# Kernel optimization log

Hardware: AMD Instinct MI355X
Metric: run time of the kernel (lower is better)

## Reference

```python
import jax, jax.numpy as jnp
import numpy as np

B, A, D, F, O, NB = 64, 1024, 5, 256, 256, 6  # batch, max_atoms, max_degree, ishape, oshape, bond feat dim


def setup_inputs() -> dict:
    key = jax.random.key(0)
    k1, k2, k3, k4 = jax.random.split(key, 4)
    atoms = jax.random.normal(k1, (B, A, F), dtype=jnp.float32)
    bonds = jax.random.normal(k2, (B, A, D, NB), dtype=jnp.float32)
    # -1 marks missing neighbor (degree padding); valid indices in [0, A)
    edges = jax.random.randint(k3, (B, A, D), -1, A)
    # xavier-normal-ish init for the 6 degree-specific weights, stacked [6, F+NB, O]
    scale = (2.0 / (F + NB + O)) ** 0.5
    degW = jax.random.normal(k4, (6, F + NB, O), dtype=jnp.float32) * scale
    b = jnp.full((1, O), 0.01, dtype=jnp.float32)
    return {"atoms": atoms, "bonds": bonds, "edges": edges, "degW": degW, "b": b}


def reference(atoms, bonds, edges, degW, b):
    # atoms: [B, A, F]; bonds: [B, A, D, NB]; edges: [B, A, D] int (-1 = pad)
    degrees = (edges != -1).sum(-1, keepdims=True)  # [B, A, 1]
    # pad a zero row at index 0 so edge -1 -> 0 gathers the mask value 0
    padded = jnp.pad(atoms, ((0, 0), (1, 0), (0, 0)))  # [B, A+1, F]
    neigh = jax.vmap(lambda p, e: p[e])(padded, edges + 1)  # [B, A, D, F]
    summed_atom = atoms + neigh.sum(axis=2)  # include_self=True
    feats = jnp.concatenate([summed_atom, bonds.sum(axis=2)], axis=-1)  # [B, A, F+NB]
    out = jnp.zeros((atoms.shape[0], atoms.shape[1], degW.shape[-1]), atoms.dtype)
    for d in range(6):  # fixed small structural loop over degree buckets
        mask = (degrees == d).astype(atoms.dtype)  # [B, A, 1]
        out = out + jax.nn.sigmoid(feats @ degW[d] + b) * mask
    return out
```

## Files before the change

### kernel.cpp

```cpp
#include <hip/hip_runtime.h>
#include <cstdint>

#define BATCH  64
#define NATOMS 1024
#define DEG    5
#define FIN    256
#define OOUT   256
#define NBF    6
#define KDIM   262
#define KP     288
#define NKT    9
#define MROWS  (BATCH * NATOMS)
#define MT     32
#define AS     296

typedef __attribute__((ext_vector_type(8))) short bf16x8;
typedef __attribute__((ext_vector_type(4))) float f32x4;

__device__ __forceinline__ unsigned short f2bf(float x) {
    unsigned u = __float_as_uint(x);
    u += 0x7fff + ((u >> 16) & 1);
    return (unsigned short)(u >> 16);
}
__device__ __forceinline__ float bf2f(unsigned short h) {
    return __uint_as_float(((unsigned)h) << 16);
}
__device__ __forceinline__ float sigmoidf_(float x) {
    return 1.f / (1.f + __expf(-x));
}

__global__ __launch_bounds__(256)
void convert_w_kernel(const float* __restrict__ degW, unsigned short* __restrict__ Wsw)
{
    const int idx = blockIdx.x * 256 + threadIdx.x;
    if (idx >= 16 * NKT * 64) return;
    const int lane = idx & 63;
    const int t    = (idx >> 6) % NKT;
    const int g    = (idx >> 6) / NKT;
    const int col  = g * 16 + (lane & 15);
    const int k0   = t * 32 + (lane >> 4) * 8;
    const float* __restrict__ W5 = degW + (size_t)DEG * KDIM * OOUT;
    unsigned short* dst = Wsw + (size_t)idx * 8;
    #pragma unroll
    for (int j = 0; j < 8; ++j) {
        const int k = k0 + j;
        dst[j] = f2bf((k < KDIM) ? W5[(size_t)k * OOUT + col] : 0.f);
    }
}

__global__ __launch_bounds__(256, 4)
void nfp_fused_kernel(const float* __restrict__ atoms, const float* __restrict__ bonds,
                      const int* __restrict__ edges, const unsigned short* __restrict__ Wsw,
                      const float* __restrict__ degW, const float* __restrict__ bias,
                      float* __restrict__ out)
{
    __shared__ short Afeat[MT * AS];
    __shared__ int   edg[MT * DEG];
    __shared__ int   deg_lds[MT];

    const int tid  = threadIdx.x;
    const int lane = tid & 63;
    const int wave = tid >> 6;

    const int bid   = blockIdx.x;
    const int xcd   = bid & 7;
    const int per   = bid >> 3;
    const int batch = (per >> 5) * 8 + xcd;
    const int blk   = per & 31;
    const int row0  = batch * NATOMS + blk * MT;

    if (tid < MT * DEG) edg[tid] = edges[row0 * DEG + tid];
    __syncthreads();
    if (tid < MT) {
        int dc = 0;
        #pragma unroll
        for (int d = 0; d < DEG; ++d) dc += (edg[tid * DEG + d] != -1) ? 1 : 0;
        deg_lds[tid] = dc;
    }

    const float* __restrict__ abase = atoms + ((size_t)batch << 10) * FIN;
    const int selfrow = blk * MT;
    #pragma unroll
    for (int c = 0; c < 4; ++c) {
        const int mb = wave * 8 + c * 2;
        float4 self[2];
        float4 nv[2][DEG];
        #pragma unroll
        for (int r = 0; r < 2; ++r) {
            const int m = mb + r;
            self[r] = *(const float4*)&abase[(size_t)(selfrow + m) * FIN + lane * 4];
            #pragma unroll
            for (int d = 0; d < DEG; ++d) {
                const int e  = edg[m * DEG + d];
                const int ei = (e >= 0) ? e : 0;
                nv[r][d] = *(const float4*)&abase[(size_t)ei * FIN + lane * 4];
            }
        }
        #pragma unroll
        for (int r = 0; r < 2; ++r) {
            const int m = mb + r;
            float4 v = self[r];
            #pragma unroll
            for (int d = 0; d < DEG; ++d) {
                const float fl = (edg[m * DEG + d] >= 0) ? 1.f : 0.f;
                v.x += fl * nv[r][d].x; v.y += fl * nv[r][d].y;
                v.z += fl * nv[r][d].z; v.w += fl * nv[r][d].w;
            }
            ushort4 us;
            us.x = f2bf(v.x); us.y = f2bf(v.y); us.z = f2bf(v.z); us.w = f2bf(v.w);
            *(ushort4*)&Afeat[m * AS + lane * 4] = us;
        }
    }
    #pragma unroll
    for (int i = lane; i < 8 * 32; i += 64) {
        const int r  = i >> 5, kk = i & 31;
        const int m  = wave * 8 + r;
        float bv = 0.f;
        if (kk < NBF) {
            const float* bb = bonds + ((size_t)row0 + m) * (DEG * NBF) + kk;
            bv = bb[0] + bb[NBF] + bb[2 * NBF] + bb[3 * NBF] + bb[4 * NBF];
        }
        Afeat[m * AS + FIN + kk] = f2bf(bv);
    }
    __syncthreads();

    const int fr = lane & 15;
    const int q  = lane >> 4;
    const int wn = wave * 64;

    f32x4 acc[2][4];
    #pragma unroll
    for (int i = 0; i < 2; ++i)
        #pragma unroll
        for (int j = 0; j < 4; ++j)
            acc[i][j] = (f32x4){0.f, 0.f, 0.f, 0.f};

    bf16x8 bcur[4], bnxt[4];
    #pragma unroll
    for (int j = 0; j < 4; ++j)
        bcur[j] = *(const bf16x8*)&Wsw[((size_t)((wave * 4 + j) * NKT) * 64 + lane) * 8];

    #pragma unroll
    for (int t = 0; t < NKT; ++t) {
        if (t + 1 < NKT) {
            #pragma unroll
            for (int j = 0; j < 4; ++j)
                bnxt[j] = *(const bf16x8*)&Wsw[((size_t)((wave * 4 + j) * NKT + t + 1) * 64 + lane) * 8];
        }
        bf16x8 af[2];
        #pragma unroll
        for (int i = 0; i < 2; ++i)
            af[i] = *(const bf16x8*)&Afeat[(i * 16 + fr) * AS + t * 32 + q * 8];
        #pragma unroll
        for (int i = 0; i < 2; ++i)
            #pragma unroll
            for (int j = 0; j < 4; ++j)
                acc[i][j] = __builtin_amdgcn_mfma_f32_16x16x32_bf16(af[i], bcur[j], acc[i][j], 0, 0, 0);
        #pragma unroll
        for (int j = 0; j < 4; ++j) bcur[j] = bnxt[j];
    }

    #pragma unroll
    for (int j = 0; j < 4; ++j) {
        const int gn = wn + j * 16 + fr;
        const float bj = bias[gn];
        #pragma unroll
        for (int i = 0; i < 2; ++i) {
            #pragma unroll
            for (int r = 0; r < 4; ++r) {
                const int lm = i * 16 + q * 4 + r;
                if (deg_lds[lm] == DEG)
                    __builtin_nontemporal_store(sigmoidf_(acc[i][j][r] + bj),
                                                &out[((size_t)row0 + lm) * OOUT + gn]);
            }
        }
    }

    for (int m = 0; m < MT; ++m) {
        const int dg = deg_lds[m];
        if (dg == DEG) continue;
        const float* __restrict__ W = degW + (size_t)dg * KDIM * OOUT;
        float s0 = 0.f, s1 = 0.f, s2 = 0.f, s3 = 0.f;
        #pragma unroll 2
        for (int k = 0; k < 260; k += 4) {
            const float w0 = W[(size_t)(k + 0) * OOUT + tid];
            const float w1 = W[(size_t)(k + 1) * OOUT + tid];
            const float w2 = W[(size_t)(k + 2) * OOUT + tid];
            const float w3 = W[(size_t)(k + 3) * OOUT + tid];
            s0 += bf2f(Afeat[m * AS + k + 0]) * w0;
            s1 += bf2f(Afeat[m * AS + k + 1]) * w1;
            s2 += bf2f(Afeat[m * AS + k + 2]) * w2;
            s3 += bf2f(Afeat[m * AS + k + 3]) * w3;
        }
        s0 += bf2f(Afeat[m * AS + 260]) * W[(size_t)260 * OOUT + tid];
        s1 += bf2f(Afeat[m * AS + 261]) * W[(size_t)261 * OOUT + tid];
        const float x = ((s0 + s1) + (s2 + s3)) + bias[tid];
        out[((size_t)row0 + m) * OOUT + tid] = sigmoidf_(x);
    }
}

#define FMT  32
#define FKT  32
#define FKPAD 288
__global__ __launch_bounds__(256, 2)
void nfp_conv_fallback(const float* __restrict__ atoms, const float* __restrict__ bonds,
                       const int* __restrict__ edges, const float* __restrict__ degW,
                       const float* __restrict__ bias, float* __restrict__ out)
{
    __shared__ float feats[FMT * FKPAD];
    __shared__ float wtile[FKT * OOUT];
    __shared__ int   edg[FMT * DEG];
    __shared__ int   deg_lds[FMT];
    __shared__ int   odd_list[FMT];
    __shared__ int   odd_cnt;
    __shared__ float b_lds[OOUT];

    const int tid = threadIdx.x, bid = blockIdx.x;
    const int batch = bid >> 5, a0 = (bid & 31) * FMT;
    const size_t atom_base = (size_t)batch * NATOMS;

    b_lds[tid] = bias[tid];
    if (tid == 0) odd_cnt = 0;
    if (tid < FMT * DEG) {
        const int m = tid / DEG, d = tid % DEG;
        edg[tid] = edges[(atom_base + a0 + m) * DEG + d];
    }
    __syncthreads();
    if (tid < FMT) {
        int dc = 0;
        #pragma unroll
        for (int d = 0; d < DEG; ++d) dc += (edg[tid * DEG + d] != -1) ? 1 : 0;
        deg_lds[tid] = dc;
        if (dc != DEG) { const int idx = atomicAdd(&odd_cnt, 1); odd_list[idx] = tid; }
    }
    __syncthreads();
    {
        const int f = tid;
        for (int m = 0; m < FMT; ++m) {
            float v = atoms[(atom_base + a0 + m) * FIN + f];
            #pragma unroll
            for (int d = 0; d < DEG; ++d) {
                const int e = edg[m * DEG + d];
                if (e >= 0) v += atoms[(atom_base + e) * FIN + f];
            }
            feats[m * FKPAD + f] = v;
        }
        #pragma unroll
        for (int t = 0; t < 4; ++t) {
            const int idx = t * 256 + tid;
            const int m = idx >> 5, kk = idx & 31;
            float v = 0.f;
            if (kk < NBF) {
                const size_t bb = (atom_base + a0 + m) * (size_t)(DEG * NBF);
                #pragma unroll
                for (int d = 0; d < DEG; ++d) v += bonds[bb + d * NBF + kk];
            }
            feats[m * FKPAD + FIN + kk] = v;
        }
    }
    const float* __restrict__ W5 = degW + (size_t)DEG * KDIM * OOUT;
    float acc[4][8];
    #pragma unroll
    for (int i = 0; i < 4; ++i)
        #pragma unroll
        for (int j = 0; j < 8; ++j) acc[i][j] = 0.f;
    const int tx = tid & 31, ty = tid >> 5;
    for (int kt = 0; kt < FKPAD; kt += FKT) {
        __syncthreads();
        #pragma unroll
        for (int t = 0; t < FKT; ++t) {
            const int k = kt + t;
            wtile[t * OOUT + tid] = (k < KDIM) ? W5[(size_t)k * OOUT + tid] : 0.f;
        }
        __syncthreads();
        #pragma unroll 4
        for (int r = 0; r < FKT; ++r) {
            float a_frag[4];
            #pragma unroll
            for (int i = 0; i < 4; ++i) a_frag[i] = feats[(ty * 4 + i) * FKPAD + kt + r];
            float w_frag[8];
            #pragma unroll
            for (int j = 0; j < 8; ++j) w_frag[j] = wtile[r * OOUT + tx + j * 32];
            #pragma unroll
            for (int i = 0; i < 4; ++i)
                #pragma unroll
                for (int j = 0; j < 8; ++j) acc[i][j] += a_frag[i] * w_frag[j];
        }
    }
    #pragma unroll
    for (int i = 0; i < 4; ++i) {
        const int m = ty * 4 + i;
        if (deg_lds[m] == DEG) {
            const size_t row = (atom_base + a0 + m) * (size_t)OOUT;
            #pragma unroll
            for (int j = 0; j < 8; ++j) {
                const int o = tx + j * 32;
                out[row + o] = sigmoidf_(acc[i][j] + b_lds[o]);
            }
        }
    }
    const int ocnt = odd_cnt;
    for (int i = 0; i < ocnt; ++i) {
        const int m = odd_list[i], d = deg_lds[m];
        const float* __restrict__ W = degW + (size_t)d * KDIM * OOUT;
        float a2 = 0.f;
        for (int k = 0; k < KDIM; ++k) a2 += feats[m * FKPAD + k] * W[(size_t)k * OOUT + tid];
        const size_t row = (atom_base + a0 + m) * (size_t)OOUT;
        out[row + tid] = sigmoidf_(a2 + b_lds[tid]);
    }
}

extern "C" void kernel_launch(void* const* d_in, const int* in_sizes, int n_in,
                              void* d_out, int out_size, void* d_ws, size_t ws_size,
                              hipStream_t stream) {
    const float* atoms = (const float*)d_in[0];
    const float* bonds = (const float*)d_in[1];
    const int*   edges = (const int*)d_in[2];
    const float* degW  = (const float*)d_in[3];
    const float* bias  = (const float*)d_in[4];
    float* out = (float*)d_out;

    const size_t WSW_BYTES = (size_t)16 * NKT * 64 * 8 * 2;

    if (ws_size < WSW_BYTES) {
        nfp_conv_fallback<<<BATCH * (NATOMS / FMT), 256, 0, stream>>>(
            atoms, bonds, edges, degW, bias, out);
        return;
    }

    unsigned short* Wsw = (unsigned short*)d_ws;
    convert_w_kernel<<<(16 * NKT * 64 + 255) / 256, 256, 0, stream>>>(degW, Wsw);
    nfp_fused_kernel<<<MROWS / MT, 256, 0, stream>>>(
        atoms, bonds, edges, Wsw, degW, bias, out);
}
```

Before: 196.0 us.

## Run non-degree-5 rows through bf16 MFMA passes with all six weight sets

Converts all six degree weight matrices into swizzled bf16 MFMA fragments when workspace allows. Tiles that contain lower-degree atoms run an extra MFMA GEMM pass per present degree, replacing the per-row scalar fp32 fallback. The A-fragment loads from shared memory are also prefetched one k-step ahead. This adds a larger conversion kernel, bf16 rounding of the lower-degree weights, and redundant full-tile GEMMs for degrees that are rare.

After: 196.5 us. Within noise of the previous version (+0.3%).

```diff
diff --git a/kernel.cpp b/kernel.cpp
--- a/kernel.cpp
+++ b/kernel.cpp
@@ -8,12 +8,13 @@
 #define OOUT   256
 #define NBF    6
 #define KDIM   262
-#define KP     288
 #define NKT    9
 #define MROWS  (BATCH * NATOMS)
 #define MT     32
 #define AS     296
 
+#define FRAG_SHORTS (16 * NKT * 64 * 8)
+
 typedef __attribute__((ext_vector_type(8))) short bf16x8;
 typedef __attribute__((ext_vector_type(4))) float f32x4;
 
@@ -30,21 +31,26 @@
 }
 
 __global__ __launch_bounds__(256)
-void convert_w_kernel(const float* __restrict__ degW, unsigned short* __restrict__ Wsw)
+void convert_w_kernel(const float* __restrict__ degW, unsigned short* __restrict__ Wsw,
+                      int all6)
 {
+    const int total = (all6 ? 6 : 1) * 16 * NKT * 64;
     const int idx = blockIdx.x * 256 + threadIdx.x;
-    if (idx >= 16 * NKT * 64) return;
+    if (idx >= total) return;
     const int lane = idx & 63;
-    const int t    = (idx >> 6) % NKT;
-    const int g    = (idx >> 6) / NKT;
+    int r = idx >> 6;
+    const int t = r % NKT; r /= NKT;
+    const int g = r & 15;
+    const int d = r >> 4;
+    const int srcd = all6 ? d : DEG;
     const int col  = g * 16 + (lane & 15);
     const int k0   = t * 32 + (lane >> 4) * 8;
-    const float* __restrict__ W5 = degW + (size_t)DEG * KDIM * OOUT;
+    const float* __restrict__ W = degW + (size_t)srcd * KDIM * OOUT;
     unsigned short* dst = Wsw + (size_t)idx * 8;
     #pragma unroll
     for (int j = 0; j < 8; ++j) {
         const int k = k0 + j;
-        dst[j] = f2bf((k < KDIM) ? W5[(size_t)k * OOUT + col] : 0.f);
+        dst[j] = f2bf((k < KDIM) ? W[(size_t)k * OOUT + col] : 0.f);
     }
 }
 
@@ -52,11 +58,12 @@
 void nfp_fused_kernel(const float* __restrict__ atoms, const float* __restrict__ bonds,
                       const int* __restrict__ edges, const unsigned short* __restrict__ Wsw,
                       const float* __restrict__ degW, const float* __restrict__ bias,
-                      float* __restrict__ out)
+                      float* __restrict__ out, int all6)
 {
     __shared__ short Afeat[MT * AS];
     __shared__ int   edg[MT * DEG];
     __shared__ int   deg_lds[MT];
+    __shared__ int   degmask;
 
     const int tid  = threadIdx.x;
     const int lane = tid & 63;
@@ -69,6 +76,7 @@
     const int blk   = per & 31;
     const int row0  = batch * NATOMS + blk * MT;
 
+    if (tid == 0) degmask = 0;
     if (tid < MT * DEG) edg[tid] = edges[row0 * DEG + tid];
     __syncthreads();
     if (tid < MT) {
@@ -76,58 +84,127 @@
         #pragma unroll
         for (int d = 0; d < DEG; ++d) dc += (edg[tid * DEG + d] != -1) ? 1 : 0;
         deg_lds[tid] = dc;
+        atomicOr(&degmask, 1 << dc);
     }
 
     const float* __restrict__ abase = atoms + ((size_t)batch << 10) * FIN;
     const int selfrow = blk * MT;
-    #pragma unroll
-    for (int c = 0; c < 4; ++c) {
-        const int mb = wave * 8 + c * 2;
-        float4 self[2];
-        float4 nv[2][DEG];
-        #pragma unroll
-        for (int r = 0; r < 2; ++r) {
-            const int m = mb + r;
-            self[r] = *(const float4*)&abase[(size_t)(selfrow + m) * FIN + lane * 4];
-            #pragma unroll
-            for (int d = 0; d < DEG; ++d) {
-                const int e  = edg[m * DEG + d];
-                const int ei = (e >= 0) ? e : 0;
-                nv[r][d] = *(const float4*)&abase[(size_t)ei * FIN + lane * 4];
-            }
-        }
-        #pragma unroll
-        for (int r = 0; r < 2; ++r) {
-            const int m = mb + r;
-            float4 v = self[r];
-            #pragma unroll
-            for (int d = 0; d < DEG; ++d) {
-                const float fl = (edg[m * DEG + d] >= 0) ? 1.f : 0.f;
-                v.x += fl * nv[r][d].x; v.y += fl * nv[r][d].y;
-                v.z += fl * nv[r][d].z; v.w += fl * nv[r][d].w;
-            }
-            ushort4 us;
-            us.x = f2bf(v.x); us.y = f2bf(v.y); us.z = f2bf(v.z); us.w = f2bf(v.w);
-            *(ushort4*)&Afeat[m * AS + lane * 4] = us;
-        }
-    }
-    #pragma unroll
-    for (int i = lane; i < 8 * 32; i += 64) {
-        const int r  = i >> 5, kk = i & 31;
-        const int m  = wave * 8 + r;
-        float bv = 0.f;
-        if (kk < NBF) {
-            const float* bb = bonds + ((size_t)row0 + m) * (DEG * NBF) + kk;
-            bv = bb[0] + bb[NBF] + bb[2 * NBF] + bb[3 * NBF] + bb[4 * NBF];
-        }
-        Afeat[m * AS + FIN + kk] = f2bf(bv);
-    }
-    __syncthreads();
-
+    const int mw = wave * 8;
+
+#define GATHER_CHUNK(MB, NR)                                                          \
+    {                                                                                 \
+        float4 self[NR]; float4 nv[NR][DEG]; int msk[NR];                             \
+        _Pragma("unroll")                                                             \
+        for (int r = 0; r < NR; ++r) {                                                \
+            const int m = (MB) + r;                                                   \
+            msk[r] = 0;                                                               \
+            self[r] = *(const float4*)&abase[(size_t)(selfrow + m) * FIN + lane * 4]; \
+            _Pragma("unroll")                                                         \
+            for (int d = 0; d < DEG; ++d) {                                           \
+                const int e = edg[m * DEG + d];                                       \
+                msk[r] |= (e >= 0) ? (1 << d) : 0;                                    \
+                const int ei = (e >= 0) ? e : 0;          \
+                nv[r][d] = *(const float4*)&abase[(size_t)ei * FIN + lane * 4];       \
+            }                                                                         \
+        }                                                                             \
+        _Pragma("unroll")                                                             \
+        for (int r = 0; r < NR; ++r) {                                                \
+            const int m = (MB) + r;                                                   \
+            float4 v = self[r];                                                       \
+            _Pragma("unroll")                                                         \
+            for (int d = 0; d < DEG; ++d) {                                           \
+                const float fl = ((msk[r] >> d) & 1) ? 1.f : 0.f;                     \
+                v.x += fl * nv[r][d].x; v.y += fl * nv[r][d].y;                       \
+                v.z += fl * nv[r][d].z; v.w += fl * nv[r][d].w;                       \
+            }                                                                         \
+            ushort4 us;                                                               \
+            us.x = f2bf(v.x); us.y = f2bf(v.y); us.z = f2bf(v.z); us.w = f2bf(v.w);   \
+            *(ushort4*)&Afeat[m * AS + lane * 4] = us;                                \
+        }                                                                             \
+    }
+
+    GATHER_CHUNK(mw + 0, 3)
+    GATHER_CHUNK(mw + 3, 3)
+    GATHER_CHUNK(mw + 6, 2)
+#undef GATHER_CHUNK
+
+    {
+        const int mz = mw + (lane >> 3), pz = lane & 7;
+        ushort4 zz = {0, 0, 0, 0};
+        *(ushort4*)&Afeat[mz * AS + FIN + pz * 4] = zz;
+        if (lane < 48) {
+            const int r  = lane / 6;
+            const int kk = lane - r * 6;
+            const int m  = mw + r;
+            const float* __restrict__ bb = bonds + ((size_t)(row0 + m)) * (DEG * NBF) + kk;
+            const float bv = bb[0] + bb[NBF] + bb[2 * NBF] + bb[3 * NBF] + bb[4 * NBF];
+            Afeat[m * AS + FIN + kk] = f2bf(bv);
+        }
+    }
+
+    const unsigned short* __restrict__ Wb5 =
+        Wsw + (all6 ? (size_t)DEG * FRAG_SHORTS : (size_t)0);
     const int fr = lane & 15;
     const int q  = lane >> 4;
     const int wn = wave * 64;
 
+    bf16x8 b0[4];
+    #pragma unroll
+    for (int j = 0; j < 4; ++j)
+        b0[j] = *(const bf16x8*)&Wb5[((size_t)((wave * 4 + j) * NKT) * 64 + lane) * 8];
+
+    __syncthreads();
+
+    auto gemm_pass = [&](const unsigned short* __restrict__ Wb, bf16x8 (&bini)[4],
+                         f32x4 (&a)[2][4]) {
+        bf16x8 bcur[4], bnxt[4], acur[2], anxt[2];
+        #pragma unroll
+        for (int j = 0; j < 4; ++j) bcur[j] = bini[j];
+        #pragma unroll
+        for (int i = 0; i < 2; ++i)
+            acur[i] = *(const bf16x8*)&Afeat[(i * 16 + fr) * AS + q * 8];
+        #pragma unroll
+        for (int t = 0; t < NKT; ++t) {
+            if (t + 1 < NKT) {
+                #pragma unroll
+                for (int j = 0; j < 4; ++j)
+                    bnxt[j] = *(const bf16x8*)&Wb[((size_t)((wave * 4 + j) * NKT + t + 1) * 64 + lane) * 8];
+                #pragma unroll
+                for (int i = 0; i < 2; ++i)
+                    anxt[i] = *(const bf16x8*)&Afeat[(i * 16 + fr) * AS + (t + 1) * 32 + q * 8];
+            }
+            #pragma unroll
+            for (int i = 0; i < 2; ++i)
+                #pragma unroll
+                for (int j = 0; j < 4; ++j)
+                    a[i][j] = __builtin_amdgcn_mfma_f32_16x16x32_bf16(acur[i], bcur[j], a[i][j], 0, 0, 0);
+            if (t + 1 < NKT) {
+                #pragma unroll
+                for (int j = 0; j < 4; ++j) bcur[j] = bnxt[j];
+                #pragma unroll
+                for (int i = 0; i < 2; ++i) acur[i] = anxt[i];
+            }
+        }
+    };
+
+    auto epilogue = [&](f32x4 (&a)[2][4], int want) {
+        #pragma unroll
+        for (int j = 0; j < 4; ++j) {
+            const int gn = wn + j * 16 + fr;
+            const float bj = bias[gn];
+            #pragma unroll
+            for (int i = 0; i < 2; ++i) {
+                #pragma unroll
+                for (int r = 0; r < 4; ++r) {
+                    const int lm = i * 16 + q * 4 + r;
+                    if (deg_lds[lm] == want)
+                        __builtin_nontemporal_store(sigmoidf_(a[i][j][r] + bj),
+                                                    &out[((size_t)row0 + lm) * OOUT + gn]);
+                }
+            }
+        }
+    };
+
     f32x4 acc[2][4];
     #pragma unroll
     for (int i = 0; i < 2; ++i)
@@ -135,67 +212,52 @@
         for (int j = 0; j < 4; ++j)
             acc[i][j] = (f32x4){0.f, 0.f, 0.f, 0.f};
 
-    bf16x8 bcur[4], bnxt[4];
-    #pragma unroll
-    for (int j = 0; j < 4; ++j)
-        bcur[j] = *(const bf16x8*)&Wsw[((size_t)((wave * 4 + j) * NKT) * 64 + lane) * 8];
-
-    #pragma unroll
-    for (int t = 0; t < NKT; ++t) {
-        if (t + 1 < NKT) {
+    gemm_pass(Wb5, b0, acc);
+    epilogue(acc, DEG);
+
+    int dmask = degmask & 0x1F;
+    if (dmask == 0) return;
+
+    if (all6) {
+        while (dmask) {
+            const int d = __ffs(dmask) - 1;
+            dmask &= dmask - 1;
+            const unsigned short* __restrict__ Wd = Wsw + (size_t)d * FRAG_SHORTS;
+            bf16x8 bd[4];
             #pragma unroll
             for (int j = 0; j < 4; ++j)
-                bnxt[j] = *(const bf16x8*)&Wsw[((size_t)((wave * 4 + j) * NKT + t + 1) * 64 + lane) * 8];
-        }
-        bf16x8 af[2];
-        #pragma unroll
-        for (int i = 0; i < 2; ++i)
-            af[i] = *(const bf16x8*)&Afeat[(i * 16 + fr) * AS + t * 32 + q * 8];
-        #pragma unroll
-        for (int i = 0; i < 2; ++i)
-            #pragma unroll
-            for (int j = 0; j < 4; ++j)
-                acc[i][j] = __builtin_amdgcn_mfma_f32_16x16x32_bf16(af[i], bcur[j], acc[i][j], 0, 0, 0);
-        #pragma unroll
-        for (int j = 0; j < 4; ++j) bcur[j] = bnxt[j];
-    }
-
-    #pragma unroll
-    for (int j = 0; j < 4; ++j) {
-        const int gn = wn + j * 16 + fr;
-        const float bj = bias[gn];
-        #pragma unroll
-        for (int i = 0; i < 2; ++i) {
-            #pragma unroll
-            for (int r = 0; r < 4; ++r) {
-                const int lm = i * 16 + q * 4 + r;
-                if (deg_lds[lm] == DEG)
-                    __builtin_nontemporal_store(sigmoidf_(acc[i][j][r] + bj),
-                                                &out[((size_t)row0 + lm) * OOUT + gn]);
-            }
-        }
-    }
-
-    for (int m = 0; m < MT; ++m) {
-        const int dg = deg_lds[m];
-        if (dg == DEG) continue;
-        const float* __restrict__ W = degW + (size_t)dg * KDIM * OOUT;
-        float s0 = 0.f, s1 = 0.f, s2 = 0.f, s3 = 0.f;
-        #pragma unroll 2
-        for (int k = 0; k < 260; k += 4) {
-            const float w0 = W[(size_t)(k + 0) * OOUT + tid];
-            const float w1 = W[(size_t)(k + 1) * OOUT + tid];
-            const float w2 = W[(size_t)(k + 2) * OOUT + tid];
-            const float w3 = W[(size_t)(k + 3) * OOUT + tid];
-            s0 += bf2f(Afeat[m * AS + k + 0]) * w0;
-            s1 += bf2f(Afeat[m * AS + k + 1]) * w1;
-            s2 += bf2f(Afeat[m * AS + k + 2]) * w2;
-            s3 += bf2f(Afeat[m * AS + k + 3]) * w3;
-        }
-        s0 += bf2f(Afeat[m * AS + 260]) * W[(size_t)260 * OOUT + tid];
-        s1 += bf2f(Afeat[m * AS + 261]) * W[(size_t)261 * OOUT + tid];
-        const float x = ((s0 + s1) + (s2 + s3)) + bias[tid];
-        out[((size_t)row0 + m) * OOUT + tid] = sigmoidf_(x);
+                bd[j] = *(const bf16x8*)&Wd[((size_t)((wave * 4 + j) * NKT) * 64 + lane) * 8];
+            f32x4 a2[2][4];
+            #pragma unroll
+            for (int i = 0; i < 2; ++i)
+                #pragma unroll
+                for (int j = 0; j < 4; ++j)
+                    a2[i][j] = (f32x4){0.f, 0.f, 0.f, 0.f};
+            gemm_pass(Wd, bd, a2);
+            epilogue(a2, d);
+        }
+    } else {
+        for (int m = 0; m < MT; ++m) {
+            const int dg = deg_lds[m];
+            if (dg == DEG) continue;
+            const float* __restrict__ W = degW + (size_t)dg * KDIM * OOUT;
+            float s0 = 0.f, s1 = 0.f, s2 = 0.f, s3 = 0.f;
+            #pragma unroll 2
+            for (int k = 0; k < 260; k += 4) {
+                const float w0 = W[(size_t)(k + 0) * OOUT + tid];
+                const float w1 = W[(size_t)(k + 1) * OOUT + tid];
+                const float w2 = W[(size_t)(k + 2) * OOUT + tid];
+                const float w3 = W[(size_t)(k + 3) * OOUT + tid];
+                s0 += bf2f(Afeat[m * AS + k + 0]) * w0;
+                s1 += bf2f(Afeat[m * AS + k + 1]) * w1;
+                s2 += bf2f(Afeat[m * AS + k + 2]) * w2;
+                s3 += bf2f(Afeat[m * AS + k + 3]) * w3;
+            }
+            s0 += bf2f(Afeat[m * AS + 260]) * W[(size_t)260 * OOUT + tid];
+            s1 += bf2f(Afeat[m * AS + 261]) * W[(size_t)261 * OOUT + tid];
+            const float x = ((s0 + s1) + (s2 + s3)) + bias[tid];
+            out[((size_t)row0 + m) * OOUT + tid] = sigmoidf_(x);
+        }
     }
 }
 
@@ -320,16 +382,21 @@
     const float* bias  = (const float*)d_in[4];
     float* out = (float*)d_out;
 
-    const size_t WSW_BYTES = (size_t)16 * NKT * 64 * 8 * 2;
-
-    if (ws_size < WSW_BYTES) {
+    const size_t WSW_ONE = (size_t)FRAG_SHORTS * 2;
+    const size_t WSW_ALL = (size_t)6 * FRAG_SHORTS * 2;
+
+    if (ws_size >= WSW_ALL) {
+        unsigned short* Wsw = (unsigned short*)d_ws;
+        convert_w_kernel<<<(6 * 16 * NKT * 64 + 255) / 256, 256, 0, stream>>>(degW, Wsw, 1);
+        nfp_fused_kernel<<<MROWS / MT, 256, 0, stream>>>(
+            atoms, bonds, edges, Wsw, degW, bias, out, 1);
+    } else if (ws_size >= WSW_ONE) {
+        unsigned short* Wsw = (unsigned short*)d_ws;
+        convert_w_kernel<<<(16 * NKT * 64 + 255) / 256, 256, 0, stream>>>(degW, Wsw, 0);
+        nfp_fused_kernel<<<MROWS / MT, 256, 0, stream>>>(
+            atoms, bonds, edges, Wsw, degW, bias, out, 0);
+    } else {
         nfp_conv_fallback<<<BATCH * (NATOMS / FMT), 256, 0, stream>>>(
             atoms, bonds, edges, degW, bias, out);
-        return;
-    }
-
-    unsigned short* Wsw = (unsigned short*)d_ws;
-    convert_w_kernel<<<(16 * NKT * 64 + 255) / 256, 256, 0, stream>>>(degW, Wsw);
-    nfp_fused_kernel<<<MROWS / MT, 256, 0, stream>>>(
-        atoms, bonds, edges, Wsw, degW, bias, out);
-}
+    }
+}
```
